# Optimization experiments

Hardware: AMD Instinct MI355X
Metric: run time of the kernel (lower is better)

Reference implementation:

```python
import jax, jax.numpy as jnp
import numpy as np

BINS = 64
VMIN, VMAX = 0.0, 1.0


def _calc_histogram(x):
    # x: [B, C, H, W] float
    B, C, H, W = x.shape
    x_norm = jnp.clip((x - VMIN) / (VMAX - VMIN), 0.0, 1.0)
    flat = x_norm.reshape(B * C, H * W)
    # torch.histc semantics over [0,1]: bin i = [i/BINS, (i+1)/BINS), last bin closed.
    idx = jnp.clip((flat * BINS).astype(jnp.int32), 0, BINS - 1)  # [B*C, HW]
    row_offset = (jnp.arange(B * C, dtype=jnp.int32) * BINS)[:, None]
    flat_idx = (idx + row_offset).reshape(-1)
    counts = jax.ops.segment_sum(
        jnp.ones(flat_idx.shape, dtype=x.dtype), flat_idx,
        num_segments=B * C * BINS,
    ).reshape(B * C, BINS)
    counts = counts / jnp.clip(counts.sum(axis=1, keepdims=True), 1e-8, None)
    return counts.reshape(B, C, BINS)


def reference(fake_images, real_images):
    hist_fake = _calc_histogram(fake_images)
    hist_real = _calc_histogram(real_images)
    # loss_type == 'l1'
    return jnp.abs(hist_fake - hist_real).mean()


def setup_inputs() -> dict:
    key = jax.random.key(0)
    k1, k2 = jax.random.split(key)
    shape = (32, 3, 512, 512)
    fake_images = jax.random.uniform(k1, shape, dtype=jnp.float32)
    real_images = jax.random.uniform(k2, shape, dtype=jnp.float32)
    return {"fake_images": fake_images, "real_images": real_images}
```

## Files before the change

kernel.cpp:

```cpp
#include <hip/hip_runtime.h>
#include <hip/hip_bf16.h>


#define HW        262144
#define ROWS      96
#define NBINS     64
#define BPR       16
#define CHUNK     (HW / BPR)
#define THREADS   256
#define V4_PER_T  (CHUNK / 4 / THREADS)
#define TOTAL_BC  (2 * ROWS * NBINS)

__global__ __launch_bounds__(THREADS)
void hist_kernel(const float* __restrict__ fake,
                 const float* __restrict__ real,
                 unsigned int* __restrict__ ghist) {
    __shared__ unsigned int h[8 * NBINS];
    const int tid = threadIdx.x;
    h[tid]       = 0u;
    h[tid + 256] = 0u;
    __syncthreads();

    const int b     = blockIdx.x;
    const int chunk = b % BPR;
    const int rowg  = b / BPR;
    const float* src = (rowg < ROWS) ? fake : real;
    const int row    = (rowg < ROWS) ? rowg : (rowg - ROWS);

    const float4* __restrict__ p =
        (const float4*)(src + (size_t)row * HW + (size_t)chunk * CHUNK);

    unsigned int* hsub = &h[(tid >> 5) * NBINS];

#pragma unroll
    for (int i = 0; i < V4_PER_T; ++i) {
        float4 v = p[i * THREADS + tid];
        int b0 = min((int)(v.x * 64.0f), 63);
        int b1 = min((int)(v.y * 64.0f), 63);
        int b2 = min((int)(v.z * 64.0f), 63);
        int b3 = min((int)(v.w * 64.0f), 63);
        atomicAdd(&hsub[b0], 1u);
        atomicAdd(&hsub[b1], 1u);
        atomicAdd(&hsub[b2], 1u);
        atomicAdd(&hsub[b3], 1u);
    }
    __syncthreads();

    if (tid < NBINS) {
        unsigned int s = 0;
#pragma unroll
        for (int k = 0; k < 8; ++k) s += h[k * NBINS + tid];
        atomicAdd(&ghist[rowg * NBINS + tid], s);
    }
}

__global__ __launch_bounds__(THREADS)
void loss_kernel(const unsigned int* __restrict__ ghist, float* __restrict__ out) {
    const int tid = threadIdx.x;
    int acc = 0;
    for (int i = tid; i < ROWS * NBINS; i += THREADS) {
        int cf = (int)ghist[i];
        int cr = (int)ghist[ROWS * NBINS + i];
        int d  = cf - cr;
        acc += (d < 0) ? -d : d;
    }
#pragma unroll
    for (int off = 32; off > 0; off >>= 1)
        acc += __shfl_down(acc, off, 64);
    __shared__ int wsum[4];
    if ((tid & 63) == 0) wsum[tid >> 6] = acc;
    __syncthreads();
    if (tid == 0) {
        int total = wsum[0] + wsum[1] + wsum[2] + wsum[3];
        out[0] = (float)((double)total / (262144.0 * (double)(ROWS * NBINS)));
    }
}

extern "C" void kernel_launch(void* const* d_in, const int* in_sizes, int n_in,
                              void* d_out, int out_size, void* d_ws, size_t ws_size,
                              hipStream_t stream) {
    const float* fake = (const float*)d_in[0];
    const float* real = (const float*)d_in[1];
    unsigned int* ghist = (unsigned int*)d_ws;
    float* out = (float*)d_out;

    hipMemsetAsync(ghist, 0, TOTAL_BC * sizeof(unsigned int), stream);

    dim3 grid(2 * ROWS * BPR);
    hist_kernel<<<grid, THREADS, 0, stream>>>(fake, real, ghist);
    loss_kernel<<<1, THREADS, 0, stream>>>(ghist, out);
}
```

Baseline: 221.7 us.

## Replace shared-memory atomic histogram with wave ballot bit-slicing and popcount

Drops the per-element LDS atomics. Each value's 6-bit bin index is broadcast across the 64-lane wave with six ballots, and lane L counts matching elements for bin L via a masked AND and popcount. Per-lane counts are reduced across the four waves in shared memory before the global atomic. This removes LDS atomic contention but adds about six ballots plus several 64-bit ALU ops per element, so the kernel may become ALU-bound instead of memory-bound.

```diff
diff --git a/kernel.cpp b/kernel.cpp
--- a/kernel.cpp
+++ b/kernel.cpp
@@ -11,15 +11,17 @@
 #define V4_PER_T  (CHUNK / 4 / THREADS)
 #define TOTAL_BC  (2 * ROWS * NBINS)
 
+__device__ __forceinline__ unsigned popc64(unsigned long long m) {
+    return __popcll(m);
+}
+
 __global__ __launch_bounds__(THREADS)
 void hist_kernel(const float* __restrict__ fake,
                  const float* __restrict__ real,
                  unsigned int* __restrict__ ghist) {
-    __shared__ unsigned int h[8 * NBINS];
-    const int tid = threadIdx.x;
-    h[tid]       = 0u;
-    h[tid + 256] = 0u;
-    __syncthreads();
+    const int tid  = threadIdx.x;
+    const int lane = tid & 63;
+    const int wave = tid >> 6;
 
     const int b     = blockIdx.x;
     const int chunk = b % BPR;
@@ -30,26 +32,39 @@
     const float4* __restrict__ p =
         (const float4*)(src + (size_t)row * HW + (size_t)chunk * CHUNK);
 
-    unsigned int* hsub = &h[(tid >> 5) * NBINS];
+    const unsigned long long x0 = (lane & 1)  ? 0ull : ~0ull;
+    const unsigned long long x1 = (lane & 2)  ? 0ull : ~0ull;
+    const unsigned long long x2 = (lane & 4)  ? 0ull : ~0ull;
+    const unsigned long long x3 = (lane & 8)  ? 0ull : ~0ull;
+    const unsigned long long x4 = (lane & 16) ? 0ull : ~0ull;
+    const unsigned long long x5 = (lane & 32) ? 0ull : ~0ull;
 
-#pragma unroll
+    unsigned cnt = 0;
+
+#pragma unroll 4
     for (int i = 0; i < V4_PER_T; ++i) {
         float4 v = p[i * THREADS + tid];
-        int b0 = min((int)(v.x * 64.0f), 63);
-        int b1 = min((int)(v.y * 64.0f), 63);
-        int b2 = min((int)(v.z * 64.0f), 63);
-        int b3 = min((int)(v.w * 64.0f), 63);
-        atomicAdd(&hsub[b0], 1u);
-        atomicAdd(&hsub[b1], 1u);
-        atomicAdd(&hsub[b2], 1u);
-        atomicAdd(&hsub[b3], 1u);
+        float c[4] = {v.x, v.y, v.z, v.w};
+#pragma unroll
+        for (int j = 0; j < 4; ++j) {
+            int bi = min((int)(c[j] * 64.0f), 63);
+            unsigned long long m0 = __ballot(bi & 1);
+            unsigned long long m1 = __ballot(bi & 2);
+            unsigned long long m2 = __ballot(bi & 4);
+            unsigned long long m3 = __ballot(bi & 8);
+            unsigned long long m4 = __ballot(bi & 16);
+            unsigned long long m5 = __ballot(bi & 32);
+            unsigned long long m = (m0 ^ x0) & (m1 ^ x1) & (m2 ^ x2)
+                                 & (m3 ^ x3) & (m4 ^ x4) & (m5 ^ x5);
+            cnt += popc64(m);
+        }
     }
+
+    __shared__ unsigned int h[4][NBINS];
+    h[wave][lane] = cnt;
     __syncthreads();
-
     if (tid < NBINS) {
-        unsigned int s = 0;
-#pragma unroll
-        for (int k = 0; k < 8; ++k) s += h[k * NBINS + tid];
+        unsigned int s = h[0][tid] + h[1][tid] + h[2][tid] + h[3][tid];
         atomicAdd(&ghist[rowg * NBINS + tid], s);
     }
 }
```

After: 230.4 us. 1.04x slower.

## Use per-thread byte histograms in LDS instead of shared atomics

Applied to the files above, without the earlier changes.

Each thread keeps a private 64-bin byte-counter histogram in LDS, padded with a 17-word pitch to spread banks. This replaces the shared-memory atomicAdd per element with plain byte increments. Each thread handles 128 values, so a byte counter cannot overflow. A wave-wise column reduction merges the per-thread counts, and each block writes its own partial histogram slice, which removes the memset and the global atomics. The loss kernel now sums the partial slices with 1024 threads, and the block count per row is halved.

```diff
diff --git a/kernel.cpp b/kernel.cpp
--- a/kernel.cpp
+++ b/kernel.cpp
@@ -5,74 +5,99 @@
 #define HW        262144
 #define ROWS      96
 #define NBINS     64
-#define BPR       16
+#define BPR       8
 #define CHUNK     (HW / BPR)
 #define THREADS   256
-#define V4_PER_T  (CHUNK / 4 / THREADS)
-#define TOTAL_BC  (2 * ROWS * NBINS)
+#define F4_ITERS  (CHUNK / 4 / THREADS)
+#define NBLOCKS   (2 * ROWS * BPR)
+#define PITCH_W   17
 
 __global__ __launch_bounds__(THREADS)
 void hist_kernel(const float* __restrict__ fake,
                  const float* __restrict__ real,
-                 unsigned int* __restrict__ ghist) {
-    __shared__ unsigned int h[8 * NBINS];
-    const int tid = threadIdx.x;
-    h[tid]       = 0u;
-    h[tid + 256] = 0u;
-    __syncthreads();
+                 unsigned int* __restrict__ partial) {
+    __shared__ unsigned int priv[THREADS * PITCH_W];
+    __shared__ unsigned int comb[4][NBINS];
+
+    const int tid  = threadIdx.x;
+    const int lane = tid & 63;
+    const int wv   = tid >> 6;
+
+#pragma unroll
+    for (int k = 0; k < PITCH_W; ++k) priv[tid * PITCH_W + k] = 0u;
 
     const int b     = blockIdx.x;
-    const int chunk = b % BPR;
-    const int rowg  = b / BPR;
+    const int chunk = b & (BPR - 1);
+    const int rowg  = b >> 3;
     const float* src = (rowg < ROWS) ? fake : real;
     const int row    = (rowg < ROWS) ? rowg : (rowg - ROWS);
 
     const float4* __restrict__ p =
         (const float4*)(src + (size_t)row * HW + (size_t)chunk * CHUNK);
 
-    unsigned int* hsub = &h[(tid >> 5) * NBINS];
+    unsigned char* my = (unsigned char*)&priv[tid * PITCH_W];
 
-#pragma unroll
-    for (int i = 0; i < V4_PER_T; ++i) {
+#pragma unroll 4
+    for (int i = 0; i < F4_ITERS; ++i) {
         float4 v = p[i * THREADS + tid];
         int b0 = min((int)(v.x * 64.0f), 63);
         int b1 = min((int)(v.y * 64.0f), 63);
         int b2 = min((int)(v.z * 64.0f), 63);
         int b3 = min((int)(v.w * 64.0f), 63);
-        atomicAdd(&hsub[b0], 1u);
-        atomicAdd(&hsub[b1], 1u);
-        atomicAdd(&hsub[b2], 1u);
-        atomicAdd(&hsub[b3], 1u);
+        my[b0]++;
+        my[b1]++;
+        my[b2]++;
+        my[b3]++;
     }
     __syncthreads();
 
+    const int cword = lane >> 2;
+    const int shift = (lane & 3) * 8;
+    unsigned cnt = 0;
+#pragma unroll 8
+    for (int t = 0; t < 64; ++t) {
+        unsigned w32 = priv[(wv * 64 + t) * PITCH_W + cword];
+        cnt += (w32 >> shift) & 0xffu;
+    }
+    comb[wv][lane] = cnt;
+    __syncthreads();
+
     if (tid < NBINS) {
-        unsigned int s = 0;
-#pragma unroll
-        for (int k = 0; k < 8; ++k) s += h[k * NBINS + tid];
-        atomicAdd(&ghist[rowg * NBINS + tid], s);
+        unsigned s = comb[0][tid] + comb[1][tid] + comb[2][tid] + comb[3][tid];
+        partial[(size_t)b * NBINS + tid] = s;
     }
 }
 
-__global__ __launch_bounds__(THREADS)
-void loss_kernel(const unsigned int* __restrict__ ghist, float* __restrict__ out) {
+__global__ __launch_bounds__(1024)
+void loss_kernel(const unsigned int* __restrict__ partial,
+                 float* __restrict__ out) {
     const int tid = threadIdx.x;
     int acc = 0;
-    for (int i = tid; i < ROWS * NBINS; i += THREADS) {
-        int cf = (int)ghist[i];
-        int cr = (int)ghist[ROWS * NBINS + i];
-        int d  = cf - cr;
+#pragma unroll
+    for (int q = 0; q < 6; ++q) {
+        const int pIdx = q * 1024 + tid;
+        const int r  = pIdx >> 6;
+        const int bb = pIdx & 63;
+        unsigned cf = 0, cr = 0;
+#pragma unroll
+        for (int c = 0; c < BPR; ++c) {
+            cf += partial[((r * BPR + c) * NBINS) + bb];
+            cr += partial[(((ROWS + r) * BPR + c) * NBINS) + bb];
+        }
+        int d = (int)cf - (int)cr;
         acc += (d < 0) ? -d : d;
     }
 #pragma unroll
     for (int off = 32; off > 0; off >>= 1)
         acc += __shfl_down(acc, off, 64);
-    __shared__ int wsum[4];
+    __shared__ int wsum[16];
     if ((tid & 63) == 0) wsum[tid >> 6] = acc;
     __syncthreads();
     if (tid == 0) {
-        int total = wsum[0] + wsum[1] + wsum[2] + wsum[3];
-        out[0] = (float)((double)total / (262144.0 * (double)(ROWS * NBINS)));
+        long long total = 0;
+#pragma unroll
+        for (int k = 0; k < 16; ++k) total += wsum[k];
+        out[0] = (float)((double)total / (262144.0 * 6144.0));
     }
 }
 
@@ -81,12 +106,9 @@
                               hipStream_t stream) {
     const float* fake = (const float*)d_in[0];
     const float* real = (const float*)d_in[1];
-    unsigned int* ghist = (unsigned int*)d_ws;
+    unsigned int* partial = (unsigned int*)d_ws;
     float* out = (float*)d_out;
 
-    hipMemsetAsync(ghist, 0, TOTAL_BC * sizeof(unsigned int), stream);
-
-    dim3 grid(2 * ROWS * BPR);
-    hist_kernel<<<grid, THREADS, 0, stream>>>(fake, real, ghist);
-    loss_kernel<<<1, THREADS, 0, stream>>>(ghist, out);
+    hist_kernel<<<NBLOCKS, THREADS, 0, stream>>>(fake, real, partial);
+    loss_kernel<<<1, 1024, 0, stream>>>(partial, out);
 }
```

Result: no change. 220.9 us (-0.4%).
